# Performance work log

Hardware: AMD Instinct MI355X
Metric: run time of the kernel (lower is better)

Reference implementation:

```python
import jax, jax.numpy as jnp
import numpy as np

B, H, S, D = 1, 16, 8192, 64
WINDOW = 1024  # window_size from init; also used as the query block size


def setup_inputs() -> dict:
    key = jax.random.key(0)
    kq, kk, kv = jax.random.split(key, 3)
    Q = jax.random.normal(kq, (B, H, S, D), dtype=jnp.float32)
    K = jax.random.normal(kk, (B, H, S, D), dtype=jnp.float32)
    V = jax.random.normal(kv, (B, H, S, D), dtype=jnp.float32)
    return {"Q": Q, "K": K, "V": V}


def _sliding_window_attn(Q, K, V, window):
    # Banded causal attention: query q attends kv with 0 <= q - kv <= window.
    # Tile queries into blocks of size W=window; each query block i only needs
    # kv positions [i*W - W, i*W + W), i.e. a 2W-wide local slice. This honors
    # the block-sparse structure instead of materializing an SxS score matrix.
    b, h, s, d = Q.shape
    W = window
    nb = s // W  # number of query blocks
    # Pad K,V by W zeros at the front so every block slice is in-bounds.
    Kp = jnp.pad(K, ((0, 0), (0, 0), (W, 0), (0, 0)))
    Vp = jnp.pad(V, ((0, 0), (0, 0), (W, 0), (0, 0)))
    # Local kv indices for each block: block i covers padded positions [i*W, i*W+2W).
    idx = jnp.arange(nb)[:, None] * W + jnp.arange(2 * W)[None, :]  # [nb, 2W]
    Kb = Kp[:, :, idx, :]  # [B,H,nb,2W,D]
    Vb = Vp[:, :, idx, :]  # [B,H,nb,2W,D]
    Qb = Q.reshape(b, h, nb, W, d)  # [B,H,nb,W,D]

    scale = np.float32(1.0 / np.sqrt(d))  # flex_attention default scaling
    scores = jnp.einsum('bhnqd,bhnkd->bhnqk', Qb, Kb) * scale  # [B,H,nb,W,2W]

    # Global positions: q_global = i*W + qi ; kv_global = i*W + kj - W.
    # Mask conds: q>=kv  <=> qi >= kj - W ;  q-kv<=W  <=> qi <= kj ; kv_global>=0.
    qi = jnp.arange(W)[:, None]          # [W,1]
    kj = jnp.arange(2 * W)[None, :]      # [1,2W]
    rel_mask = (qi <= kj) & (qi >= kj - W)                        # [W,2W]
    kv_global = jnp.arange(nb)[:, None, None] * W + kj[None] - W  # [nb,1,2W]
    mask = rel_mask[None] & (kv_global >= 0)                      # [nb,W,2W]

    neg = jnp.finfo(scores.dtype).min
    scores = jnp.where(mask[None, None], scores, neg)
    attn = jax.nn.softmax(scores, axis=-1)
    out = jnp.einsum('bhnqk,bhnkd->bhnqd', attn, Vb)
    return out.reshape(b, h, s, d)


def reference(Q, K, V):
    return _sliding_window_attn(Q, K, V, WINDOW)
```

## Files before the change

kernel.cpp:

```cpp
#include <hip/hip_runtime.h>
#include <stdint.h>

namespace {
constexpr int kH = 16;
constexpr int kS = 8192;
constexpr int kD = 64;
constexpr int kW = 1024;

typedef __attribute__((ext_vector_type(4)))  float float4_t;
typedef __attribute__((ext_vector_type(16))) float f32x16;
typedef __attribute__((ext_vector_type(8)))  short bf16x8;
typedef __attribute__((ext_vector_type(8)))  short short8_t;

__device__ __forceinline__ unsigned short f2bf(float f) {
    union { float fv; uint32_t u; } c; c.fv = f;
    return (unsigned short)((c.u + 0x7fffu + ((c.u >> 16) & 1u)) >> 16);
}

__device__ __forceinline__ float fexp2(float x) {
#if __has_builtin(__builtin_amdgcn_exp2f)
    return __builtin_amdgcn_exp2f(x);
#else
    return exp2f(x);
#endif
}

__device__ __forceinline__ void gload16(const void* g, char* l) {
    __builtin_amdgcn_global_load_lds(
        (const __attribute__((address_space(1))) void*)g,
        (__attribute__((address_space(3))) void*)l, 16, 0, 0);
}

__global__ __launch_bounds__(256)
void prep_kv(const float* __restrict__ K, const float* __restrict__ V,
             unsigned short* __restrict__ Kb, unsigned short* __restrict__ Vt) {
    __shared__ float tile[64][65];
    const int h  = blockIdx.y;
    const int s0 = blockIdx.x * 64;
    const int tid = threadIdx.x;
    const size_t hb = (size_t)h * kS * kD;

    {
        const size_t base = hb + (size_t)s0 * kD + (size_t)tid * 16;
        float4_t a = *(const float4_t*)(K + base);
        float4_t b = *(const float4_t*)(K + base + 4);
        float4_t c = *(const float4_t*)(K + base + 8);
        float4_t d = *(const float4_t*)(K + base + 12);
        short8_t o0, o1;
        #pragma unroll
        for (int j = 0; j < 4; ++j) {
            o0[j] = (short)f2bf(a[j]); o0[j + 4] = (short)f2bf(b[j]);
            o1[j] = (short)f2bf(c[j]); o1[j + 4] = (short)f2bf(d[j]);
        }
        *(short8_t*)(Kb + base)     = o0;
        *(short8_t*)(Kb + base + 8) = o1;
    }

    #pragma unroll
    for (int it = 0; it < 4; ++it) {
        const int n = tid + it * 256;
        const int s = n >> 4, d0 = (n & 15) * 4;
        float4_t v = *(const float4_t*)(V + hb + (size_t)(s0 + s) * kD + d0);
        tile[s][d0 + 0] = v[0]; tile[s][d0 + 1] = v[1];
        tile[s][d0 + 2] = v[2]; tile[s][d0 + 3] = v[3];
    }
    __syncthreads();
    #pragma unroll
    for (int it = 0; it < 2; ++it) {
        const int n = tid + it * 256;
        const int d = n >> 3, sc = (n & 7) * 8;
        short8_t o;
        #pragma unroll
        for (int j = 0; j < 8; ++j) o[j] = (short)f2bf(tile[sc + j][d]);
        *(short8_t*)(Vt + (size_t)h * kD * kS + (size_t)d * kS + s0 + sc) = o;
    }
}

__global__ __launch_bounds__(512, 2)
void swa_main(const float* __restrict__ Qg, const unsigned short* __restrict__ Kb,
              const unsigned short* __restrict__ Vt, float* __restrict__ Og) {
    __shared__ __align__(16) char lds[2][16384];

    const int lid  = blockIdx.x;
    const int swz  = (lid & 7) * 64 + (lid >> 3);
    const int h    = swz >> 5;
    const int qblk = swz & 31;

    const int tid  = threadIdx.x;
    const int wv   = tid >> 6;
    const int lane = tid & 63;
    const int lq   = lane & 31;
    const int hi   = lane >> 5;

    const int q0b = qblk * 256;
    const int qs  = q0b + wv * 32;
    const int q   = qs + lq;
    const size_t hb  = (size_t)h * kS * kD;
    const size_t hbv = (size_t)h * kD * kS;

    constexpr float qscale = 0.125f * 1.44269504f;
    bf16x8 qf[4];
    {
        const float* qp = Qg + hb + (size_t)q * kD + hi * 8;
        #pragma unroll
        for (int c = 0; c < 4; ++c) {
            float4_t a = *(const float4_t*)(qp + c * 16);
            float4_t b = *(const float4_t*)(qp + c * 16 + 4);
            bf16x8 f;
            #pragma unroll
            for (int j = 0; j < 4; ++j) {
                f[j]     = (short)f2bf(a[j] * qscale);
                f[j + 4] = (short)f2bf(b[j] * qscale);
            }
            qf[c] = f;
        }
    }

    f32x16 acc[2], lsum;
    #pragma unroll
    for (int r = 0; r < 16; ++r) { acc[0][r] = 0.f; acc[1][r] = 0.f; lsum[r] = 0.f; }

    bf16x8 ones;
    #pragma unroll
    for (int j = 0; j < 8; ++j) ones[j] = (short)0x3F80;

    const int kstart = (q0b >= kW) ? q0b - kW : 0;
    const int nt     = (q0b + 256 - kstart) >> 6;

    int srcK, srcV;
    {
        const int c = tid ^ ((tid >> 3) & 7);
        srcK = (c >> 3) * 64 + (c & 7) * 8;
        srcV = (c >> 3) * kS + (c & 7) * 8;
    }
    const unsigned short* KbH = Kb + hb;
    const unsigned short* VtH = Vt + hbv;

    auto stage = [&](int buf, int kb) {
        gload16(KbH + (size_t)kb * 64 + srcK, &lds[buf][tid * 16]);
        gload16(VtH + kb + srcV,              &lds[buf][8192 + tid * 16]);
    };

    stage(0, kstart);
    for (int t = 0; t < nt; ++t) {
        const int kb  = kstart + t * 64;
        const int kbn = (t + 1 < nt) ? kb + 64 : kb;
        stage((t + 1) & 1, kbn);
        asm volatile("s_waitcnt vmcnt(2)" ::: "memory");
        __builtin_amdgcn_s_barrier();
        asm volatile("" ::: "memory");

        const char* Kl = lds[t & 1];
        const char* Vl = lds[t & 1] + 8192;

        #pragma unroll
        for (int half = 0; half < 2; ++half) {
            const int kh = kb + half * 32;
            if (kh <= qs && kh >= qs - kW) {
                const int krow = half * 32 + lq;
                const int ksw  = (lq & 7) << 4;
                bf16x8 kf[4];
                #pragma unroll
                for (int c = 0; c < 4; ++c)
                    kf[c] = *(const bf16x8*)(Kl + ((krow * 128 + c * 32 + hi * 16) ^ ksw));

                f32x16 st;
                #pragma unroll
                for (int r = 0; r < 16; ++r) st[r] = 0.f;
                __builtin_amdgcn_s_setprio(1);
                #pragma unroll
                for (int c = 0; c < 4; ++c)
                    st = __builtin_amdgcn_mfma_f32_32x32x16_bf16(kf[c], qf[c], st, 0, 0, 0);
                __builtin_amdgcn_s_setprio(0);

                bf16x8 vf[4];
                #pragma unroll
                for (int dh = 0; dh < 2; ++dh)
                    #pragma unroll
                    for (int kc = 0; kc < 2; ++kc)
                        vf[dh * 2 + kc] = *(const bf16x8*)(
                            Vl + (((dh * 32 + lq) * 128 + half * 64 + kc * 32 + hi * 16) ^ ksw));

                float p[16];
                const bool interior = (kh <= qs - 32) && (kh >= qs - 992);
                if (interior) {
                    #pragma unroll
                    for (int r = 0; r < 16; ++r) p[r] = fexp2(st[r]);
                } else {
                    #pragma unroll
                    for (int r = 0; r < 16; ++r) {
                        const int ki = kh + (r & 3) + 8 * (r >> 2) + 4 * hi;
                        const bool ok = (ki <= q) && (ki + kW >= q);
                        const float e = fexp2(st[r]);
                        p[r] = ok ? e : 0.f;
                    }
                }

                unsigned int wrd[8];
                #pragma unroll
                for (int j = 0; j < 8; ++j)
                    asm("v_cvt_pk_bf16_f32 %0, %1, %2" : "=v"(wrd[j]) : "v"(p[2 * j]), "v"(p[2 * j + 1]));
                asm("v_permlane32_swap_b32 %0, %1" : "+v"(wrd[0]), "+v"(wrd[2]));
                asm("v_permlane32_swap_b32 %0, %1" : "+v"(wrd[1]), "+v"(wrd[3]));
                asm("v_permlane32_swap_b32 %0, %1" : "+v"(wrd[4]), "+v"(wrd[6]));
                asm("v_permlane32_swap_b32 %0, %1" : "+v"(wrd[5]), "+v"(wrd[7]));
                union U { unsigned int u[4]; bf16x8 v; };
                U u0, u1;
                u0.u[0] = wrd[0]; u0.u[1] = wrd[1]; u0.u[2] = wrd[2]; u0.u[3] = wrd[3];
                u1.u[0] = wrd[4]; u1.u[1] = wrd[5]; u1.u[2] = wrd[6]; u1.u[3] = wrd[7];

                __builtin_amdgcn_s_setprio(1);
                acc[0] = __builtin_amdgcn_mfma_f32_32x32x16_bf16(vf[0], u0.v, acc[0], 0, 0, 0);
                acc[1] = __builtin_amdgcn_mfma_f32_32x32x16_bf16(vf[2], u0.v, acc[1], 0, 0, 0);
                lsum   = __builtin_amdgcn_mfma_f32_32x32x16_bf16(ones,  u0.v, lsum,   0, 0, 0);
                acc[0] = __builtin_amdgcn_mfma_f32_32x32x16_bf16(vf[1], u1.v, acc[0], 0, 0, 0);
                acc[1] = __builtin_amdgcn_mfma_f32_32x32x16_bf16(vf[3], u1.v, acc[1], 0, 0, 0);
                lsum   = __builtin_amdgcn_mfma_f32_32x32x16_bf16(ones,  u1.v, lsum,   0, 0, 0);
                __builtin_amdgcn_s_setprio(0);
            }
        }

        asm volatile("" ::: "memory");
        __builtin_amdgcn_s_barrier();
        asm volatile("" ::: "memory");
    }

    const float rl = 1.f / lsum[0];
    float* op = Og + hb + (size_t)q * kD;
    #pragma unroll
    for (int g = 0; g < 4; ++g) {
        float4_t o0, o1;
        #pragma unroll
        for (int j = 0; j < 4; ++j) {
            o0[j] = acc[0][g * 4 + j] * rl;
            o1[j] = acc[1][g * 4 + j] * rl;
        }
        *(float4_t*)(op + g * 8 + hi * 4)      = o0;
        *(float4_t*)(op + 32 + g * 8 + hi * 4) = o1;
    }
}
}

extern "C" void kernel_launch(void* const* d_in, const int* in_sizes, int n_in,
                              void* d_out, int out_size, void* d_ws, size_t ws_size,
                              hipStream_t stream) {
    (void)in_sizes; (void)n_in; (void)out_size; (void)ws_size;
    const float* Q = (const float*)d_in[0];
    const float* K = (const float*)d_in[1];
    const float* V = (const float*)d_in[2];
    float* O = (float*)d_out;
    unsigned short* Kb = (unsigned short*)d_ws;
    unsigned short* Vt = Kb + (size_t)kH * kS * kD;

    prep_kv<<<dim3(kS / 64, kH), dim3(256), 0, stream>>>(K, V, Kb, Vt);
    swa_main<<<dim3(512), dim3(512), 0, stream>>>(Q, Kb, Vt, O);
}
```

Before: 79.72 us.

## Switch attention to 16x16x32 MFMA tiles with smaller query blocks and pre-tiled K/V

The attention kernel now processes 64-query blocks with 256 threads (16 queries per wave) and 32-key tiles, using 16x16x32 bf16 MFMAs instead of 32x32x16. The prep kernel writes K and transposed V into a pre-tiled layout so each tile is one contiguous chunk that loads straight into LDS without swizzling. The row sum is now accumulated in registers and reduced with shuffles instead of an extra MFMA against ones. The grid grows to 2048 blocks with occupancy hint 6 to raise parallelism and cut wasted masked work at block edges. In exchange, K/V tiles are reloaded more often per query and each tile needs extra shuffles to relayout P.

Result: no change. 80.87 us (+1.4%).

```diff
diff --git a/kernel.cpp b/kernel.cpp
--- a/kernel.cpp
+++ b/kernel.cpp
@@ -8,7 +8,7 @@
 constexpr int kW = 1024;
 
 typedef __attribute__((ext_vector_type(4)))  float float4_t;
-typedef __attribute__((ext_vector_type(16))) float f32x16;
+typedef __attribute__((ext_vector_type(4)))  float f32x4;
 typedef __attribute__((ext_vector_type(8)))  short bf16x8;
 typedef __attribute__((ext_vector_type(8)))  short short8_t;
 
@@ -35,27 +35,33 @@
 void prep_kv(const float* __restrict__ K, const float* __restrict__ V,
              unsigned short* __restrict__ Kb, unsigned short* __restrict__ Vt) {
     __shared__ float tile[64][65];
-    const int h  = blockIdx.y;
-    const int s0 = blockIdx.x * 64;
+    const int h   = blockIdx.y;
+    const int tix = blockIdx.x;
+    const int s0  = tix * 64;
     const int tid = threadIdx.x;
     const size_t hb = (size_t)h * kS * kD;
-
-    {
-        const size_t base = hb + (size_t)s0 * kD + (size_t)tid * 16;
-        float4_t a = *(const float4_t*)(K + base);
-        float4_t b = *(const float4_t*)(K + base + 4);
-        float4_t c = *(const float4_t*)(K + base + 8);
-        float4_t d = *(const float4_t*)(K + base + 12);
-        short8_t o0, o1;
-        #pragma unroll
-        for (int j = 0; j < 4; ++j) {
-            o0[j] = (short)f2bf(a[j]); o0[j + 4] = (short)f2bf(b[j]);
-            o1[j] = (short)f2bf(c[j]); o1[j + 4] = (short)f2bf(d[j]);
-        }
-        *(short8_t*)(Kb + base)     = o0;
-        *(short8_t*)(Kb + base + 8) = o1;
-    }
-
+    unsigned short* Ko = Kb + hb + (size_t)tix * 4096;
+    unsigned short* Vo = Vt + hb + (size_t)tix * 4096;
+
+    #pragma unroll
+    for (int it = 0; it < 4; ++it) {
+        const int n = tid + it * 256;
+        const int s = n >> 4, d0 = (n & 15) * 4;
+        float4_t v = *(const float4_t*)(K + hb + (size_t)(s0 + s) * kD + d0);
+        tile[s][d0 + 0] = v[0]; tile[s][d0 + 1] = v[1];
+        tile[s][d0 + 2] = v[2]; tile[s][d0 + 3] = v[3];
+    }
+    __syncthreads();
+    #pragma unroll
+    for (int i = 0; i < 2; ++i) {
+        const int n = tid + i * 256;
+        const int tt = n >> 8, g = (n >> 5) & 7, rr = n & 31;
+        short8_t o;
+        #pragma unroll
+        for (int j = 0; j < 8; ++j) o[j] = (short)f2bf(tile[tt * 32 + rr][g * 8 + j]);
+        *(short8_t*)(Ko + n * 8) = o;
+    }
+    __syncthreads();
     #pragma unroll
     for (int it = 0; it < 4; ++it) {
         const int n = tid + it * 256;
@@ -66,158 +72,153 @@
     }
     __syncthreads();
     #pragma unroll
-    for (int it = 0; it < 2; ++it) {
-        const int n = tid + it * 256;
-        const int d = n >> 3, sc = (n & 7) * 8;
+    for (int i = 0; i < 2; ++i) {
+        const int n = tid + i * 256;
+        const int tt = n >> 8, g = (n >> 6) & 3, d = n & 63;
         short8_t o;
         #pragma unroll
-        for (int j = 0; j < 8; ++j) o[j] = (short)f2bf(tile[sc + j][d]);
-        *(short8_t*)(Vt + (size_t)h * kD * kS + (size_t)d * kS + s0 + sc) = o;
-    }
-}
-
-__global__ __launch_bounds__(512, 2)
+        for (int j = 0; j < 8; ++j) o[j] = (short)f2bf(tile[tt * 32 + g * 8 + j][d]);
+        *(short8_t*)(Vo + n * 8) = o;
+    }
+}
+
+__global__ __launch_bounds__(256, 6)
 void swa_main(const float* __restrict__ Qg, const unsigned short* __restrict__ Kb,
               const unsigned short* __restrict__ Vt, float* __restrict__ Og) {
-    __shared__ __align__(16) char lds[2][16384];
+    __shared__ __align__(16) char lds[2][8192];
 
     const int lid  = blockIdx.x;
-    const int swz  = (lid & 7) * 64 + (lid >> 3);
-    const int h    = swz >> 5;
-    const int qblk = swz & 31;
+    const int swz  = (lid & 7) * 256 + (lid >> 3);
+    const int h    = swz >> 7;
+    const int qblk = swz & 127;
 
     const int tid  = threadIdx.x;
     const int wv   = tid >> 6;
     const int lane = tid & 63;
-    const int lq   = lane & 31;
-    const int hi   = lane >> 5;
-
-    const int q0b = qblk * 256;
-    const int qs  = q0b + wv * 32;
-    const int q   = qs + lq;
-    const size_t hb  = (size_t)h * kS * kD;
-    const size_t hbv = (size_t)h * kD * kS;
+    const int lq   = lane & 15;
+    const int a    = lane >> 4;
+
+    const int q0b = qblk * 64;
+    const int qs  = q0b + wv * 16;
+    const int qg  = qs + lq;
+    const size_t hb = (size_t)h * kS * kD;
 
     constexpr float qscale = 0.125f * 1.44269504f;
-    bf16x8 qf[4];
+    bf16x8 qf[2];
     {
-        const float* qp = Qg + hb + (size_t)q * kD + hi * 8;
-        #pragma unroll
-        for (int c = 0; c < 4; ++c) {
-            float4_t a = *(const float4_t*)(qp + c * 16);
-            float4_t b = *(const float4_t*)(qp + c * 16 + 4);
+        const float* qp = Qg + hb + (size_t)qg * kD + a * 8;
+        #pragma unroll
+        for (int c = 0; c < 2; ++c) {
+            float4_t x = *(const float4_t*)(qp + c * 32);
+            float4_t y = *(const float4_t*)(qp + c * 32 + 4);
             bf16x8 f;
             #pragma unroll
             for (int j = 0; j < 4; ++j) {
-                f[j]     = (short)f2bf(a[j] * qscale);
-                f[j + 4] = (short)f2bf(b[j] * qscale);
+                f[j]     = (short)f2bf(x[j] * qscale);
+                f[j + 4] = (short)f2bf(y[j] * qscale);
             }
             qf[c] = f;
         }
     }
 
-    f32x16 acc[2], lsum;
-    #pragma unroll
-    for (int r = 0; r < 16; ++r) { acc[0][r] = 0.f; acc[1][r] = 0.f; lsum[r] = 0.f; }
-
-    bf16x8 ones;
-    #pragma unroll
-    for (int j = 0; j < 8; ++j) ones[j] = (short)0x3F80;
+    f32x4 acc[4];
+    #pragma unroll
+    for (int d = 0; d < 4; ++d)
+        #pragma unroll
+        for (int r = 0; r < 4; ++r) acc[d][r] = 0.f;
+    float lp = 0.f;
 
     const int kstart = (q0b >= kW) ? q0b - kW : 0;
-    const int nt     = (q0b + 256 - kstart) >> 6;
-
-    int srcK, srcV;
-    {
-        const int c = tid ^ ((tid >> 3) & 7);
-        srcK = (c >> 3) * 64 + (c & 7) * 8;
-        srcV = (c >> 3) * kS + (c & 7) * 8;
-    }
+    const int nt     = (q0b + 64 - kstart) >> 5;
+
     const unsigned short* KbH = Kb + hb;
-    const unsigned short* VtH = Vt + hbv;
+    const unsigned short* VtH = Vt + hb;
 
     auto stage = [&](int buf, int kb) {
-        gload16(KbH + (size_t)kb * 64 + srcK, &lds[buf][tid * 16]);
-        gload16(VtH + kb + srcV,              &lds[buf][8192 + tid * 16]);
+        const unsigned short* Kt = KbH + (size_t)(kb >> 5) * 2048;
+        const unsigned short* Vq = VtH + (size_t)(kb >> 5) * 2048;
+        const int db = wv * 1024;
+        gload16(Kt + tid * 8, &lds[buf][db]);
+        gload16(Vq + tid * 8, &lds[buf][4096 + db]);
     };
+
+    const int kbase = lq * 16 + a * 512;
+    const int vbase = 4096 + lq * 16 + a * 1024;
+    union U { unsigned int u[4]; bf16x8 v; };
 
     stage(0, kstart);
     for (int t = 0; t < nt; ++t) {
-        const int kb  = kstart + t * 64;
-        const int kbn = (t + 1 < nt) ? kb + 64 : kb;
+        const int kb  = kstart + t * 32;
+        const int kbn = (t + 1 < nt) ? kb + 32 : kb;
         stage((t + 1) & 1, kbn);
         asm volatile("s_waitcnt vmcnt(2)" ::: "memory");
         __builtin_amdgcn_s_barrier();
         asm volatile("" ::: "memory");
 
-        const char* Kl = lds[t & 1];
-        const char* Vl = lds[t & 1] + 8192;
-
-        #pragma unroll
-        for (int half = 0; half < 2; ++half) {
-            const int kh = kb + half * 32;
-            if (kh <= qs && kh >= qs - kW) {
-                const int krow = half * 32 + lq;
-                const int ksw  = (lq & 7) << 4;
-                bf16x8 kf[4];
+        const char* B = lds[t & 1];
+        const bool active = (kb <= qs + 15) && (kb + 31 >= qs - kW);
+        if (active) {
+            bf16x8 kf00 = *(const bf16x8*)(B + kbase);
+            bf16x8 kf01 = *(const bf16x8*)(B + kbase + 2048);
+            bf16x8 kf10 = *(const bf16x8*)(B + kbase + 256);
+            bf16x8 kf11 = *(const bf16x8*)(B + kbase + 2304);
+
+            f32x4 st0, st1;
+            #pragma unroll
+            for (int r = 0; r < 4; ++r) { st0[r] = 0.f; st1[r] = 0.f; }
+            __builtin_amdgcn_s_setprio(1);
+            st0 = __builtin_amdgcn_mfma_f32_16x16x32_bf16(kf00, qf[0], st0, 0, 0, 0);
+            st1 = __builtin_amdgcn_mfma_f32_16x16x32_bf16(kf10, qf[0], st1, 0, 0, 0);
+            st0 = __builtin_amdgcn_mfma_f32_16x16x32_bf16(kf01, qf[1], st0, 0, 0, 0);
+            st1 = __builtin_amdgcn_mfma_f32_16x16x32_bf16(kf11, qf[1], st1, 0, 0, 0);
+            __builtin_amdgcn_s_setprio(0);
+
+            bf16x8 vf0 = *(const bf16x8*)(B + vbase);
+            bf16x8 vf1 = *(const bf16x8*)(B + vbase + 256);
+            bf16x8 vf2 = *(const bf16x8*)(B + vbase + 512);
+            bf16x8 vf3 = *(const bf16x8*)(B + vbase + 768);
+
+            float p[8];
+            const bool fast = (kb + 31 <= qs) && (kb >= qs + 15 - kW);
+            if (fast) {
                 #pragma unroll
-                for (int c = 0; c < 4; ++c)
-                    kf[c] = *(const bf16x8*)(Kl + ((krow * 128 + c * 32 + hi * 16) ^ ksw));
-
-                f32x16 st;
+                for (int r = 0; r < 4; ++r) { p[r] = fexp2(st0[r]); p[4 + r] = fexp2(st1[r]); }
+            } else {
                 #pragma unroll
-                for (int r = 0; r < 16; ++r) st[r] = 0.f;
-                __builtin_amdgcn_s_setprio(1);
-                #pragma unroll
-                for (int c = 0; c < 4; ++c)
-                    st = __builtin_amdgcn_mfma_f32_32x32x16_bf16(kf[c], qf[c], st, 0, 0, 0);
-                __builtin_amdgcn_s_setprio(0);
-
-                bf16x8 vf[4];
-                #pragma unroll
-                for (int dh = 0; dh < 2; ++dh)
-                    #pragma unroll
-                    for (int kc = 0; kc < 2; ++kc)
-                        vf[dh * 2 + kc] = *(const bf16x8*)(
-                            Vl + (((dh * 32 + lq) * 128 + half * 64 + kc * 32 + hi * 16) ^ ksw));
-
-                float p[16];
-                const bool interior = (kh <= qs - 32) && (kh >= qs - 992);
-                if (interior) {
-                    #pragma unroll
-                    for (int r = 0; r < 16; ++r) p[r] = fexp2(st[r]);
-                } else {
-                    #pragma unroll
-                    for (int r = 0; r < 16; ++r) {
-                        const int ki = kh + (r & 3) + 8 * (r >> 2) + 4 * hi;
-                        const bool ok = (ki <= q) && (ki + kW >= q);
-                        const float e = fexp2(st[r]);
-                        p[r] = ok ? e : 0.f;
-                    }
+                for (int r = 0; r < 4; ++r) {
+                    const int k0 = kb + a * 4 + r;
+                    const int k1 = k0 + 16;
+                    p[r]     = ((k0 <= qg) && (k0 + kW >= qg)) ? fexp2(st0[r]) : 0.f;
+                    p[4 + r] = ((k1 <= qg) && (k1 + kW >= qg)) ? fexp2(st1[r]) : 0.f;
                 }
-
-                unsigned int wrd[8];
-                #pragma unroll
-                for (int j = 0; j < 8; ++j)
-                    asm("v_cvt_pk_bf16_f32 %0, %1, %2" : "=v"(wrd[j]) : "v"(p[2 * j]), "v"(p[2 * j + 1]));
-                asm("v_permlane32_swap_b32 %0, %1" : "+v"(wrd[0]), "+v"(wrd[2]));
-                asm("v_permlane32_swap_b32 %0, %1" : "+v"(wrd[1]), "+v"(wrd[3]));
-                asm("v_permlane32_swap_b32 %0, %1" : "+v"(wrd[4]), "+v"(wrd[6]));
-                asm("v_permlane32_swap_b32 %0, %1" : "+v"(wrd[5]), "+v"(wrd[7]));
-                union U { unsigned int u[4]; bf16x8 v; };
-                U u0, u1;
-                u0.u[0] = wrd[0]; u0.u[1] = wrd[1]; u0.u[2] = wrd[2]; u0.u[3] = wrd[3];
-                u1.u[0] = wrd[4]; u1.u[1] = wrd[5]; u1.u[2] = wrd[6]; u1.u[3] = wrd[7];
-
-                __builtin_amdgcn_s_setprio(1);
-                acc[0] = __builtin_amdgcn_mfma_f32_32x32x16_bf16(vf[0], u0.v, acc[0], 0, 0, 0);
-                acc[1] = __builtin_amdgcn_mfma_f32_32x32x16_bf16(vf[2], u0.v, acc[1], 0, 0, 0);
-                lsum   = __builtin_amdgcn_mfma_f32_32x32x16_bf16(ones,  u0.v, lsum,   0, 0, 0);
-                acc[0] = __builtin_amdgcn_mfma_f32_32x32x16_bf16(vf[1], u1.v, acc[0], 0, 0, 0);
-                acc[1] = __builtin_amdgcn_mfma_f32_32x32x16_bf16(vf[3], u1.v, acc[1], 0, 0, 0);
-                lsum   = __builtin_amdgcn_mfma_f32_32x32x16_bf16(ones,  u1.v, lsum,   0, 0, 0);
-                __builtin_amdgcn_s_setprio(0);
             }
+            #pragma unroll
+            for (int r = 0; r < 8; ++r) lp += p[r];
+
+            unsigned int x0, x1, y0, y1;
+            asm("v_cvt_pk_bf16_f32 %0, %1, %2" : "=v"(x0) : "v"(p[0]), "v"(p[1]));
+            asm("v_cvt_pk_bf16_f32 %0, %1, %2" : "=v"(x1) : "v"(p[2]), "v"(p[3]));
+            asm("v_cvt_pk_bf16_f32 %0, %1, %2" : "=v"(y0) : "v"(p[4]), "v"(p[5]));
+            asm("v_cvt_pk_bf16_f32 %0, %1, %2" : "=v"(y1) : "v"(p[6]), "v"(p[7]));
+            asm("v_permlane32_swap_b32 %0, %1" : "+v"(x0), "+v"(y0));
+            asm("v_permlane32_swap_b32 %0, %1" : "+v"(x1), "+v"(y1));
+            const unsigned int s0 = (unsigned int)__shfl_xor((int)y0, 16);
+            const unsigned int s1 = (unsigned int)__shfl_xor((int)y1, 16);
+            const unsigned int t0 = (unsigned int)__shfl_xor((int)x0, 16);
+            const unsigned int t1 = (unsigned int)__shfl_xor((int)x1, 16);
+            const bool hb16 = (lane & 16) != 0;
+            U u;
+            u.u[0] = hb16 ? s0 : x0;
+            u.u[1] = hb16 ? s1 : x1;
+            u.u[2] = hb16 ? y0 : t0;
+            u.u[3] = hb16 ? y1 : t1;
+
+            __builtin_amdgcn_s_setprio(1);
+            acc[0] = __builtin_amdgcn_mfma_f32_16x16x32_bf16(vf0, u.v, acc[0], 0, 0, 0);
+            acc[1] = __builtin_amdgcn_mfma_f32_16x16x32_bf16(vf1, u.v, acc[1], 0, 0, 0);
+            acc[2] = __builtin_amdgcn_mfma_f32_16x16x32_bf16(vf2, u.v, acc[2], 0, 0, 0);
+            acc[3] = __builtin_amdgcn_mfma_f32_16x16x32_bf16(vf3, u.v, acc[3], 0, 0, 0);
+            __builtin_amdgcn_s_setprio(0);
         }
 
         asm volatile("" ::: "memory");
@@ -225,18 +226,16 @@
         asm volatile("" ::: "memory");
     }
 
-    const float rl = 1.f / lsum[0];
-    float* op = Og + hb + (size_t)q * kD;
-    #pragma unroll
-    for (int g = 0; g < 4; ++g) {
-        float4_t o0, o1;
-        #pragma unroll
-        for (int j = 0; j < 4; ++j) {
-            o0[j] = acc[0][g * 4 + j] * rl;
-            o1[j] = acc[1][g * 4 + j] * rl;
-        }
-        *(float4_t*)(op + g * 8 + hi * 4)      = o0;
-        *(float4_t*)(op + 32 + g * 8 + hi * 4) = o1;
+    lp += __shfl_xor(lp, 16);
+    lp += __shfl_xor(lp, 32);
+    const float rl = 1.f / lp;
+    float* op = Og + hb + (size_t)qg * kD;
+    #pragma unroll
+    for (int d = 0; d < 4; ++d) {
+        float4_t o;
+        #pragma unroll
+        for (int r = 0; r < 4; ++r) o[r] = acc[d][r] * rl;
+        *(float4_t*)(op + d * 16 + a * 4) = o;
     }
 }
 }
@@ -253,5 +252,5 @@
     unsigned short* Vt = Kb + (size_t)kH * kS * kD;
 
     prep_kv<<<dim3(kS / 64, kH), dim3(256), 0, stream>>>(K, V, Kb, Vt);
-    swa_main<<<dim3(512), dim3(512), 0, stream>>>(Q, Kb, Vt, O);
-}
+    swa_main<<<dim3(2048), dim3(256), 0, stream>>>(Q, Kb, Vt, O);
+}
```
